# Optimization experiments

Hardware: AMD Instinct MI355X
Metric: run time of the kernel (lower is better)

Reference implementation:

```python
import jax, jax.numpy as jnp
import numpy as np

TEMPERATURE = 1.0
N_ITER = 3
B, N_PATTERNS, N_NEURONS = 4096, 8192, 1024


def setup_inputs() -> dict:
    key = jax.random.key(0)
    kx, kp = jax.random.split(key)
    x = jax.random.normal(kx, (B, N_NEURONS), dtype=jnp.float32)
    # patterns initialized as tanh(randn * initial_variance) in the original module
    patterns = jnp.tanh(jax.random.normal(kp, (N_PATTERNS, N_NEURONS), dtype=jnp.float32) * 0.1)
    return {"x": x, "patterns": patterns}


def reference(x, patterns):
    # Iterative Hopfield update: x <- softmax(T * x @ P^T) @ P, repeated N_ITER times.
    def body(carry, _):
        scores = TEMPERATURE * jnp.einsum('bn,pn->bp', carry, patterns)  # [B, P]
        new_x = jnp.einsum('bp,pn->bn', jax.nn.softmax(scores, axis=1), patterns)  # [B, N]
        return new_x, None
    x, _ = jax.lax.scan(body, x, None, length=N_ITER)
    return x
```

## Files before the change

kernel.cpp:

```cpp
#include <hip/hip_runtime.h>
#include <hip/hip_fp16.h>
#include <stdint.h>

#define B_ROWS 4096
#define N_PAT  8192
#define N_NEU  1024

typedef _Float16 f16x8 __attribute__((ext_vector_type(8)));
typedef _Float16 f16x4 __attribute__((ext_vector_type(4)));
typedef float    f32x4 __attribute__((ext_vector_type(4)));

__global__ __launch_bounds__(256) void convert_f32_f16(
    const float* __restrict__ in, _Float16* __restrict__ out, int n4) {
  int idx    = blockIdx.x * 256 + threadIdx.x;
  int stride = gridDim.x * 256;
  for (int i = idx; i < n4; i += stride) {
    float4 v = reinterpret_cast<const float4*>(in)[i];
    f16x4 h  = { (_Float16)v.x, (_Float16)v.y, (_Float16)v.z, (_Float16)v.w };
    reinterpret_cast<f16x4*>(out)[i] = h;
  }
}

__global__ __launch_bounds__(256) void transpose_f32_f16(
    const float* __restrict__ in, _Float16* __restrict__ out, int rows, int cols) {
  __shared__ float tile[32][33];
  int c0 = blockIdx.x * 32, r0 = blockIdx.y * 32;
  int tx = threadIdx.x, ty = threadIdx.y;
  #pragma unroll
  for (int i = 0; i < 32; i += 8)
    tile[ty + i][tx] = in[(size_t)(r0 + ty + i) * cols + c0 + tx];
  __syncthreads();
  #pragma unroll
  for (int i = 0; i < 32; i += 8)
    out[(size_t)(c0 + ty + i) * rows + r0 + tx] = (_Float16)tile[tx][ty + i];
}

__device__ __forceinline__ void gload_lds16(const _Float16* g, _Float16* l) {
  __builtin_amdgcn_global_load_lds(
      (const __attribute__((address_space(1))) uint32_t*)g,
      (__attribute__((address_space(3))) uint32_t*)l, 16, 0, 0);
}

template <typename OUT_T>
__global__ __launch_bounds__(256, 4) void gemm_bt_db(
    const _Float16* __restrict__ A, const _Float16* __restrict__ Bt,
    OUT_T* __restrict__ C, int M, int N, int K, int KS) {
  __shared__ _Float16 As[2][128 * 32];
  __shared__ _Float16 Bs[2][128 * 32];
  const int t    = threadIdx.x;
  const int lane = t & 63;
  const int w    = t >> 6;
  const int wr   = w >> 1;
  const int wc   = w & 1;
  const int m0   = blockIdx.x * 128;
  const int n0   = blockIdx.y * 128;
  const int k0   = blockIdx.z * KS;

  const int srow = w * 16 + (lane >> 2);
  const int scol = (lane & 3) * 8;
  const _Float16* gA = A  + (size_t)(m0 + srow) * K + scol + k0;
  const _Float16* gB = Bt + (size_t)(n0 + srow) * K + scol + k0;
  const size_t jump = (size_t)64 * K;

  const int lrow = lane & 15;
  const int kg   = lane >> 4;
  const int nt   = KS / 32;

  f32x4 acc[4][4] = {};

  {
    _Float16* lA = &As[0][w * 512];
    _Float16* lB = &Bs[0][w * 512];
    gload_lds16(gA, lA);
    gload_lds16(gA + jump, lA + 2048);
    gload_lds16(gB, lB);
    gload_lds16(gB + jump, lB + 2048);
  }
  __syncthreads();

  for (int it = 0; it < nt; ++it) {
    const int cur = it & 1;
    if (it + 1 < nt) {
      const int kt = (it + 1) * 32;
      _Float16* lA = &As[cur ^ 1][w * 512];
      _Float16* lB = &Bs[cur ^ 1][w * 512];
      gload_lds16(gA + kt, lA);
      gload_lds16(gA + jump + kt, lA + 2048);
      gload_lds16(gB + kt, lB);
      gload_lds16(gB + jump + kt, lB + 2048);
    }

    f16x8 af[4], bf[4];
    #pragma unroll
    for (int mi = 0; mi < 4; ++mi)
      af[mi] = *reinterpret_cast<const f16x8*>(&As[cur][(wr * 64 + mi * 16 + lrow) * 32 + kg * 8]);
    #pragma unroll
    for (int ni = 0; ni < 4; ++ni)
      bf[ni] = *reinterpret_cast<const f16x8*>(&Bs[cur][(wc * 64 + ni * 16 + lrow) * 32 + kg * 8]);
    #pragma unroll
    for (int mi = 0; mi < 4; ++mi) {
      #pragma unroll
      for (int ni = 0; ni < 4; ++ni)
        acc[mi][ni] = __builtin_amdgcn_mfma_f32_16x16x32_f16(af[mi], bf[ni], acc[mi][ni], 0, 0, 0);
    }
    __syncthreads();
  }

  OUT_T* Cz = C + (size_t)blockIdx.z * M * N;
  const int crow = (lane >> 4) * 4;
  const int ccol = lane & 15;
  #pragma unroll
  for (int mi = 0; mi < 4; ++mi) {
    #pragma unroll
    for (int ni = 0; ni < 4; ++ni) {
      #pragma unroll
      for (int r = 0; r < 4; ++r) {
        int row = m0 + wr * 64 + mi * 16 + crow + r;
        int col = n0 + wc * 64 + ni * 16 + ccol;
        Cz[(size_t)row * N + col] = (OUT_T)acc[mi][ni][r];
      }
    }
  }
}

template <typename OUT_T, int SPLIT>
__global__ __launch_bounds__(256) void reduce_partials(
    const float* __restrict__ Cp, OUT_T* __restrict__ out, int n4, int stride4) {
  int idx    = blockIdx.x * 256 + threadIdx.x;
  int stride = gridDim.x * 256;
  for (int i = idx; i < n4; i += stride) {
    float4 a = reinterpret_cast<const float4*>(Cp)[i];
    #pragma unroll
    for (int s = 1; s < SPLIT; ++s) {
      float4 b = reinterpret_cast<const float4*>(Cp)[(size_t)s * stride4 + i];
      a.x += b.x; a.y += b.y; a.z += b.z; a.w += b.w;
    }
    if constexpr (sizeof(OUT_T) == 2) {
      f16x4 h = { (_Float16)a.x, (_Float16)a.y, (_Float16)a.z, (_Float16)a.w };
      reinterpret_cast<f16x4*>(out)[i] = h;
    } else {
      reinterpret_cast<float4*>(out)[i] = a;
    }
  }
}

__global__ __launch_bounds__(256) void softmax_rows(_Float16* __restrict__ S, int N) {
  const int t = threadIdx.x;
  f16x8* pv = reinterpret_cast<f16x8*>(S + (size_t)blockIdx.x * N);
  float v[32];
  float m = -3.0e38f;
  #pragma unroll
  for (int i = 0; i < 4; ++i) {
    f16x8 h = pv[i * 256 + t];
    #pragma unroll
    for (int e = 0; e < 8; ++e) {
      float f = (float)h[e];
      v[i * 8 + e] = f;
      m = fmaxf(m, f);
    }
  }
  #pragma unroll
  for (int o = 32; o; o >>= 1) m = fmaxf(m, __shfl_xor(m, o));
  __shared__ float redm[4];
  if ((t & 63) == 0) redm[t >> 6] = m;
  __syncthreads();
  m = fmaxf(fmaxf(redm[0], redm[1]), fmaxf(redm[2], redm[3]));

  float s = 0.f;
  #pragma unroll
  for (int i = 0; i < 32; ++i) { v[i] = __expf(v[i] - m); s += v[i]; }
  #pragma unroll
  for (int o = 32; o; o >>= 1) s += __shfl_xor(s, o);
  __shared__ float reds[4];
  if ((t & 63) == 0) reds[t >> 6] = s;
  __syncthreads();
  s = reds[0] + reds[1] + reds[2] + reds[3];
  const float inv = 1.0f / s;

  #pragma unroll
  for (int i = 0; i < 4; ++i) {
    f16x8 h;
    #pragma unroll
    for (int e = 0; e < 8; ++e) h[e] = (_Float16)(v[i * 8 + e] * inv);
    pv[i * 256 + t] = h;
  }
}

extern "C" void kernel_launch(void* const* d_in, const int* in_sizes, int n_in,
                              void* d_out, int out_size, void* d_ws, size_t ws_size,
                              hipStream_t stream) {
  const float* x        = (const float*)d_in[0];
  const float* patterns = (const float*)d_in[1];
  float* out            = (float*)d_out;
  char* ws = (char*)d_ws;

  _Float16* Xb   = (_Float16*)(ws);
  _Float16* Pb   = (_Float16*)(ws + ((size_t)8  << 20));
  _Float16* PbT  = (_Float16*)(ws + ((size_t)24 << 20));
  _Float16* S    = (_Float16*)(ws + ((size_t)40 << 20));
  float*    part = (float*)   (ws + ((size_t)104 << 20));

  const size_t base = (size_t)104 << 20;
  const int split = (ws_size >= base + ((size_t)64 << 20)) ? 4
                  : (ws_size >= base + ((size_t)32 << 20)) ? 2 : 1;

  convert_f32_f16<<<dim3(1024), dim3(256), 0, stream>>>(x, Xb, (B_ROWS * N_NEU) / 4);
  convert_f32_f16<<<dim3(2048), dim3(256), 0, stream>>>(patterns, Pb, (N_PAT * N_NEU) / 4);
  transpose_f32_f16<<<dim3(N_NEU / 32, N_PAT / 32), dim3(32, 8), 0, stream>>>(patterns, PbT, N_PAT, N_NEU);

  const int n4 = (B_ROWS * N_NEU) / 4;
  const int stride4 = n4;

  for (int it = 0; it < 3; ++it) {
    gemm_bt_db<_Float16><<<dim3(B_ROWS / 128, N_PAT / 128, 1), dim3(256), 0, stream>>>(
        Xb, Pb, S, B_ROWS, N_PAT, N_NEU, N_NEU);
    softmax_rows<<<dim3(B_ROWS), dim3(256), 0, stream>>>(S, N_PAT);

    if (split > 1) {
      gemm_bt_db<float><<<dim3(B_ROWS / 128, N_NEU / 128, split), dim3(256), 0, stream>>>(
          S, PbT, part, B_ROWS, N_NEU, N_PAT, N_PAT / split);
      if (it < 2) {
        if (split == 4)
          reduce_partials<_Float16, 4><<<dim3(2048), dim3(256), 0, stream>>>(part, Xb, n4, stride4);
        else
          reduce_partials<_Float16, 2><<<dim3(2048), dim3(256), 0, stream>>>(part, Xb, n4, stride4);
      } else {
        if (split == 4)
          reduce_partials<float, 4><<<dim3(2048), dim3(256), 0, stream>>>(part, out, n4, stride4);
        else
          reduce_partials<float, 2><<<dim3(2048), dim3(256), 0, stream>>>(part, out, n4, stride4);
      }
    } else {
      gemm_bt_db<float><<<dim3(B_ROWS / 128, N_NEU / 128, 1), dim3(256), 0, stream>>>(
          S, PbT, part, B_ROWS, N_NEU, N_PAT, N_PAT);
      if (it < 2)
        reduce_partials<_Float16, 1><<<dim3(2048), dim3(256), 0, stream>>>(part, Xb, n4, stride4);
      else
        reduce_partials<float, 1><<<dim3(2048), dim3(256), 0, stream>>>(part, out, n4, stride4);
    }
  }
}
```

Before: 617.7 us.

## Replace score GEMM with 256x256-tile, 8-wave, swizzled-LDS pipelined kernel

Swaps the first GEMM (X @ P^T) for a new kernel that uses 256x256 output tiles with 8 waves, a K-step of 64, XOR-swizzled LDS layout to avoid bank conflicts, and a two-stage prefetch with explicit vmcnt waits, barriers and setprio around the MFMA bursts. The larger tile raises arithmetic intensity and cuts global traffic per FLOP. It aims to keep the matrix cores busier than the old 128x128 double-buffered kernel. In exchange it uses 128 KB of LDS and more accumulator registers per thread, which limits occupancy. It also launches far fewer blocks (16x32).

```diff
diff --git a/kernel.cpp b/kernel.cpp
--- a/kernel.cpp
+++ b/kernel.cpp
@@ -9,6 +9,10 @@
 typedef _Float16 f16x8 __attribute__((ext_vector_type(8)));
 typedef _Float16 f16x4 __attribute__((ext_vector_type(4)));
 typedef float    f32x4 __attribute__((ext_vector_type(4)));
+
+__device__ __forceinline__ f32x4 mfma16(f16x8 a, f16x8 b, f32x4 c) {
+  return __builtin_amdgcn_mfma_f32_16x16x32_f16(a, b, c, 0, 0, 0);
+}
 
 __global__ __launch_bounds__(256) void convert_f32_f16(
     const float* __restrict__ in, _Float16* __restrict__ out, int n4) {
@@ -39,6 +43,117 @@
   __builtin_amdgcn_global_load_lds(
       (const __attribute__((address_space(1))) uint32_t*)g,
       (__attribute__((address_space(3))) uint32_t*)l, 16, 0, 0);
+}
+
+__global__ __launch_bounds__(512, 2) void gemm1_8p(
+    const _Float16* __restrict__ A, const _Float16* __restrict__ Bt,
+    _Float16* __restrict__ C, int M, int N, int K) {
+  __shared__ _Float16 lds[2][2][256 * 64];
+  const int t    = threadIdx.x;
+  const int lane = t & 63;
+  const int w    = t >> 6;
+  const int wr   = w >> 2;
+  const int wc   = w & 3;
+  const int m0   = blockIdx.x * 256;
+  const int n0   = blockIdx.y * 256;
+
+  const int srow  = w * 8 + (lane >> 3);
+  const int sgran = ((lane & 7) ^ ((lane >> 3) & 7)) * 8;
+  const _Float16* gA = A  + (size_t)(m0 + srow) * K + sgran;
+  const _Float16* gB = Bt + (size_t)(n0 + srow) * K + sgran;
+  const size_t rj = (size_t)64 * K;
+  const int ldst  = w * 512;
+
+  const int lrow = lane & 15;
+  const int kg   = lane >> 4;
+  const int NT   = K >> 6;
+
+  f32x4 acc[8][4] = {};
+
+  #pragma unroll
+  for (int j = 0; j < 4; ++j) {
+    gload_lds16(gA + j * rj,      &lds[0][0][j * 4096 + ldst]);
+    gload_lds16(gB + j * rj,      &lds[0][1][j * 4096 + ldst]);
+  }
+  #pragma unroll
+  for (int j = 0; j < 4; ++j) {
+    gload_lds16(gA + j * rj + 64, &lds[1][0][j * 4096 + ldst]);
+    gload_lds16(gB + j * rj + 64, &lds[1][1][j * 4096 + ldst]);
+  }
+  asm volatile("s_waitcnt vmcnt(8)" ::: "memory");
+  __builtin_amdgcn_s_barrier();
+  __builtin_amdgcn_sched_barrier(0);
+
+  for (int tt = 0; tt < NT; ++tt) {
+    const int s = tt & 1;
+    const _Float16* As = lds[s][0];
+    const _Float16* Bs = lds[s][1];
+
+    f16x8 bf[4][2];
+    #pragma unroll
+    for (int ni = 0; ni < 4; ++ni) {
+      const int br = wc * 64 + ni * 16 + lrow;
+      #pragma unroll
+      for (int ks = 0; ks < 2; ++ks)
+        bf[ni][ks] = *reinterpret_cast<const f16x8*>(
+            &Bs[br * 64 + (((ks * 4 + kg) ^ (br & 7)) * 8)]);
+    }
+
+    #pragma unroll
+    for (int p = 0; p < 4; ++p) {
+      f16x8 af[2][2];
+      #pragma unroll
+      for (int j = 0; j < 2; ++j) {
+        const int ar = wr * 128 + (p * 2 + j) * 16 + lrow;
+        #pragma unroll
+        for (int ks = 0; ks < 2; ++ks)
+          af[j][ks] = *reinterpret_cast<const f16x8*>(
+              &As[ar * 64 + (((ks * 4 + kg) ^ (ar & 7)) * 8)]);
+      }
+      __builtin_amdgcn_s_setprio(1);
+      #pragma unroll
+      for (int j = 0; j < 2; ++j) {
+        #pragma unroll
+        for (int ni = 0; ni < 4; ++ni) {
+          acc[p * 2 + j][ni] = mfma16(af[j][0], bf[ni][0], acc[p * 2 + j][ni]);
+          acc[p * 2 + j][ni] = mfma16(af[j][1], bf[ni][1], acc[p * 2 + j][ni]);
+        }
+      }
+      __builtin_amdgcn_s_setprio(0);
+      if (p < 3) __builtin_amdgcn_s_barrier();
+    }
+
+    __builtin_amdgcn_s_barrier();
+    __builtin_amdgcn_sched_barrier(0);
+    if (tt + 2 < NT) {
+      const int kt = (tt + 2) * 64;
+      #pragma unroll
+      for (int j = 0; j < 4; ++j) {
+        gload_lds16(gA + j * rj + kt, &lds[s][0][j * 4096 + ldst]);
+        gload_lds16(gB + j * rj + kt, &lds[s][1][j * 4096 + ldst]);
+      }
+      asm volatile("s_waitcnt vmcnt(8)" ::: "memory");
+    } else {
+      asm volatile("s_waitcnt vmcnt(0)" ::: "memory");
+    }
+    __builtin_amdgcn_s_barrier();
+    __builtin_amdgcn_sched_barrier(0);
+  }
+
+  const int crow = (lane >> 4) * 4;
+  const int ccol = lane & 15;
+  #pragma unroll
+  for (int mi = 0; mi < 8; ++mi) {
+    #pragma unroll
+    for (int ni = 0; ni < 4; ++ni) {
+      #pragma unroll
+      for (int r = 0; r < 4; ++r) {
+        int row = m0 + wr * 128 + mi * 16 + crow + r;
+        int col = n0 + wc * 64 + ni * 16 + ccol;
+        C[(size_t)row * N + col] = (_Float16)acc[mi][ni][r];
+      }
+    }
+  }
 }
 
 template <typename OUT_T>
@@ -212,8 +327,8 @@
   const int stride4 = n4;
 
   for (int it = 0; it < 3; ++it) {
-    gemm_bt_db<_Float16><<<dim3(B_ROWS / 128, N_PAT / 128, 1), dim3(256), 0, stream>>>(
-        Xb, Pb, S, B_ROWS, N_PAT, N_NEU, N_NEU);
+    gemm1_8p<<<dim3(B_ROWS / 256, N_PAT / 256), dim3(512), 0, stream>>>(
+        Xb, Pb, S, B_ROWS, N_PAT, N_NEU);
     softmax_rows<<<dim3(B_ROWS), dim3(256), 0, stream>>>(S, N_PAT);
 
     if (split > 1) {
```

Result: faster. 592.4 us (-4.1%).
